# Kernel optimization log

Hardware: AMD Instinct MI355X
Metric: run time of the kernel (lower is better)

The kernel has to match this reference:

```python
import jax, jax.numpy as jnp
import numpy as np

VOC_SIZE = 100000
EMB_SIZE = 300
BATCH = 262144


def setup_inputs() -> dict:
    key = jax.random.key(0)
    k1, k2, k3, k4, k5, k6, k7, k8 = jax.random.split(key, 8)
    center = jax.random.randint(k1, (BATCH, 1), 0, VOC_SIZE)
    outside = jax.random.randint(k2, (BATCH, 1), 0, VOC_SIZE)
    coocs = jax.random.uniform(k3, (BATCH, 1), dtype=jnp.float32)
    weighting = jax.random.uniform(k4, (BATCH, 1), dtype=jnp.float32)
    center_embedding = jax.random.normal(k5, (VOC_SIZE, EMB_SIZE), dtype=jnp.float32)
    outside_embedding = jax.random.normal(k6, (VOC_SIZE, EMB_SIZE), dtype=jnp.float32)
    center_bias = jax.random.normal(k7, (VOC_SIZE, 1), dtype=jnp.float32)
    outside_bias = jax.random.normal(k8, (VOC_SIZE, 1), dtype=jnp.float32)
    return {
        "center": center,
        "outside": outside,
        "coocs": coocs,
        "weighting": weighting,
        "center_embedding": center_embedding,
        "outside_embedding": outside_embedding,
        "center_bias": center_bias,
        "outside_bias": outside_bias,
    }


def reference(center, outside, coocs, weighting,
              center_embedding, outside_embedding,
              center_bias, outside_bias):
    c_idx = center[:, 0]    # [B]
    o_idx = outside[:, 0]   # [B]
    center_embeds = center_embedding[c_idx]     # [B, E]
    outside_embeds = outside_embedding[o_idx]   # [B, E]
    c_bias = center_bias[c_idx]                 # [B, 1]
    o_bias = outside_bias[o_idx]                # [B, 1]
    # per-sample dot product, keepdims to match [B, 1]
    inner = jnp.sum(center_embeds * outside_embeds, axis=-1, keepdims=True)  # [B, 1]
    err = inner + c_bias + o_bias - coocs
    loss = jnp.sum(weighting * err * err)
    return loss
```

## Files before the change

### kernel.cpp

```cpp
#include <hip/hip_runtime.h>

#define BATCH 262144
#define EMB 300
#define NBLK 4096
#define WPB 4

__global__ __launch_bounds__(256) void glove_main(
    const int*   __restrict__ center,
    const int*   __restrict__ outside,
    const float* __restrict__ coocs,
    const float* __restrict__ weighting,
    const float* __restrict__ cemb,
    const float* __restrict__ oemb,
    const float* __restrict__ cbias,
    const float* __restrict__ obias,
    float*       __restrict__ block_sums)
{
    const int tid  = threadIdx.x;
    const int warp = tid >> 6;
    const int lane = tid & 63;
    const int l    = lane & 15;
    const int g    = lane >> 4;
    const int base = (blockIdx.x * WPB + warp) * 16 + g;

    int ci[4], oi[4];
    #pragma unroll
    for (int it = 0; it < 4; ++it) {
        ci[it] = center[base + it * 4];
        oi[it] = outside[base + it * 4];
    }

    float4 sa[2][5], sb[2][5];
    float  scb[2], sob[2], scc[2], swt[2];

    #pragma unroll
    for (int s = 0; s < 2; ++s) {
        const float4* __restrict__ A = (const float4*)(cemb + (long)ci[s] * EMB);
        const float4* __restrict__ B = (const float4*)(oemb + (long)oi[s] * EMB);
        #pragma unroll
        for (int i = 0; i < 4; ++i) {
            sa[s][i] = A[i * 16 + l];
            sb[s][i] = B[i * 16 + l];
        }
        sa[s][4].x = 0.f; sa[s][4].y = 0.f; sa[s][4].z = 0.f; sa[s][4].w = 0.f;
        sb[s][4] = sa[s][4];
        if (l < 11) {
            sa[s][4] = A[64 + l];
            sb[s][4] = B[64 + l];
        }
        scb[s] = cbias[ci[s]];
        sob[s] = obias[oi[s]];
        scc[s] = coocs[base + s * 4];
        swt[s] = weighting[base + s * 4];
    }

    float local = 0.0f;

    #pragma unroll
    for (int it = 0; it < 4; ++it) {
        const int buf = it & 1;

        float s = 0.f;
        #pragma unroll
        for (int i = 0; i < 5; ++i) {
            s += sa[buf][i].x * sb[buf][i].x + sa[buf][i].y * sb[buf][i].y
               + sa[buf][i].z * sb[buf][i].z + sa[buf][i].w * sb[buf][i].w;
        }
        const float cbv = scb[buf], obv = sob[buf], ccv = scc[buf], wtv = swt[buf];

        if (it + 2 < 4) {
            const int n = it + 2;
            const float4* __restrict__ A = (const float4*)(cemb + (long)ci[n] * EMB);
            const float4* __restrict__ B = (const float4*)(oemb + (long)oi[n] * EMB);
            #pragma unroll
            for (int i = 0; i < 4; ++i) {
                sa[buf][i] = A[i * 16 + l];
                sb[buf][i] = B[i * 16 + l];
            }
            if (l < 11) {
                sa[buf][4] = A[64 + l];
                sb[buf][4] = B[64 + l];
            } else {
                sa[buf][4].x = 0.f; sa[buf][4].y = 0.f; sa[buf][4].z = 0.f; sa[buf][4].w = 0.f;
                sb[buf][4] = sa[buf][4];
            }
            scb[buf] = cbias[ci[n]];
            sob[buf] = obias[oi[n]];
            scc[buf] = coocs[base + n * 4];
            swt[buf] = weighting[base + n * 4];
        }

        s += __shfl_xor(s, 1);
        s += __shfl_xor(s, 2);
        s += __shfl_xor(s, 4);
        s += __shfl_xor(s, 8);

        if (l == 0) {
            const float e = s + cbv + obv - ccv;
            local += wtv * e * e;
        }
    }

    local += __shfl_down(local, 32, 64);
    local += __shfl_down(local, 16, 64);

    __shared__ float smem[WPB];
    if (lane == 0) smem[warp] = local;
    __syncthreads();
    if (tid == 0)
        block_sums[blockIdx.x] = smem[0] + smem[1] + smem[2] + smem[3];
}

__global__ __launch_bounds__(1024) void glove_reduce(
    const float* __restrict__ part, float* __restrict__ out)
{
    const int t = threadIdx.x;
    float4 v = ((const float4*)part)[t];
    float s = v.x + v.y + v.z + v.w;
    #pragma unroll
    for (int off = 32; off > 0; off >>= 1)
        s += __shfl_down(s, off, 64);
    __shared__ float sm[16];
    if ((t & 63) == 0) sm[t >> 6] = s;
    __syncthreads();
    if (t < 16) {
        float x = sm[t];
        #pragma unroll
        for (int off = 8; off > 0; off >>= 1)
            x += __shfl_down(x, off, 16);
        if (t == 0) out[0] = x;
    }
}

extern "C" void kernel_launch(void* const* d_in, const int* in_sizes, int n_in,
                              void* d_out, int out_size, void* d_ws, size_t ws_size,
                              hipStream_t stream) {
    const int*   center    = (const int*)  d_in[0];
    const int*   outside   = (const int*)  d_in[1];
    const float* coocs     = (const float*)d_in[2];
    const float* weighting = (const float*)d_in[3];
    const float* cemb      = (const float*)d_in[4];
    const float* oemb      = (const float*)d_in[5];
    const float* cbias     = (const float*)d_in[6];
    const float* obias     = (const float*)d_in[7];
    float* out        = (float*)d_out;
    float* block_sums = (float*)d_ws;

    glove_main<<<NBLK, 256, 0, stream>>>(
        center, outside, coocs, weighting, cemb, oemb, cbias, obias, block_sums);
    glove_reduce<<<1, 1024, 0, stream>>>(block_sums, out);
}
```

Measured before the change: 302.8 us.

## Bucket-sort samples by center index to improve embedding gather locality

Adds a histogram, scan and atomic scatter pass that builds a permutation grouping samples by center-index bucket (128 rows per bucket). The main kernel then processes samples in that order, so center-embedding rows are likely reused from cache instead of being fetched randomly from DRAM. Each per-pair loss is written back to its original position and summed in original order, which keeps the reduction order fixed. In exchange it adds several extra launches, contended atomics within a bucket, and indirect loads of the index, cooc and weighting arrays. The outside-embedding gathers stay random.

Result: slower. 431.8 us (+42.6%).

```diff
diff --git a/kernel.cpp b/kernel.cpp
--- a/kernel.cpp
+++ b/kernel.cpp
@@ -2,8 +2,191 @@
 
 #define BATCH 262144
 #define EMB 300
+#define VOC 100000
 #define NBLK 4096
 #define WPB 4
+
+#define BSHIFT 7
+#define NBUCKET ((VOC + (1 << BSHIFT) - 1) >> BSHIFT)
+
+#define WS_BLOCKSUMS 0
+#define WS_HIST      16384
+#define WS_OFFS      20480
+#define WS_PERM      24576
+#define WS_PLOSS     (24576 + 1048576)
+#define WS_NEED      (WS_PLOSS + 1048576)
+
+__global__ __launch_bounds__(256) void glove_hist(
+    const int* __restrict__ center, int* __restrict__ hist)
+{
+    const int i = blockIdx.x * 256 + threadIdx.x;
+    atomicAdd(&hist[center[i] >> BSHIFT], 1);
+}
+
+__global__ __launch_bounds__(1024) void glove_scan(
+    const int* __restrict__ hist, int* __restrict__ offs)
+{
+    const int t = threadIdx.x;
+    int v = (t < NBUCKET) ? hist[t] : 0;
+    const int orig = v;
+
+    #pragma unroll
+    for (int off = 1; off < 64; off <<= 1) {
+        int n = __shfl_up(v, off, 64);
+        if ((t & 63) >= off) v += n;
+    }
+    __shared__ int wsums[16];
+    if ((t & 63) == 63) wsums[t >> 6] = v;
+    __syncthreads();
+    if (t < 16) {
+        int w = wsums[t];
+        #pragma unroll
+        for (int off = 1; off < 16; off <<= 1) {
+            int n = __shfl_up(w, off, 16);
+            if (t >= off) w += n;
+        }
+        wsums[t] = w;
+    }
+    __syncthreads();
+    const int add = (t >= 64) ? wsums[(t >> 6) - 1] : 0;
+    if (t < NBUCKET) offs[t] = (v + add) - orig;
+}
+
+__global__ __launch_bounds__(256) void glove_scatter(
+    const int* __restrict__ center, int* __restrict__ offs,
+    int* __restrict__ perm)
+{
+    const int i = blockIdx.x * 256 + threadIdx.x;
+    const int b = center[i] >> BSHIFT;
+    const int slot = atomicAdd(&offs[b], 1);
+    perm[slot] = i;
+}
+
+__global__ __launch_bounds__(256) void glove_main_perm(
+    const int*   __restrict__ perm,
+    const int*   __restrict__ center,
+    const int*   __restrict__ outside,
+    const float* __restrict__ coocs,
+    const float* __restrict__ weighting,
+    const float* __restrict__ cemb,
+    const float* __restrict__ oemb,
+    const float* __restrict__ cbias,
+    const float* __restrict__ obias,
+    float*       __restrict__ pair_loss)
+{
+    const int tid  = threadIdx.x;
+    const int warp = tid >> 6;
+    const int lane = tid & 63;
+    const int l    = lane & 15;
+    const int g    = lane >> 4;
+    const int base = (blockIdx.x * WPB + warp) * 16 + g;
+
+    int pp[4];
+    #pragma unroll
+    for (int it = 0; it < 4; ++it) pp[it] = perm[base + it * 4];
+
+    int ci[4], oi[4];
+    #pragma unroll
+    for (int it = 0; it < 4; ++it) {
+        ci[it] = center[pp[it]];
+        oi[it] = outside[pp[it]];
+    }
+
+    float4 sa[2][5], sb[2][5];
+    float  scb[2], sob[2], scc[2], swt[2];
+
+    #pragma unroll
+    for (int s = 0; s < 2; ++s) {
+        const float4* __restrict__ A = (const float4*)(cemb + (long)ci[s] * EMB);
+        const float4* __restrict__ B = (const float4*)(oemb + (long)oi[s] * EMB);
+        #pragma unroll
+        for (int i = 0; i < 4; ++i) {
+            sa[s][i] = A[i * 16 + l];
+            sb[s][i] = B[i * 16 + l];
+        }
+        sa[s][4].x = 0.f; sa[s][4].y = 0.f; sa[s][4].z = 0.f; sa[s][4].w = 0.f;
+        sb[s][4] = sa[s][4];
+        if (l < 11) {
+            sa[s][4] = A[64 + l];
+            sb[s][4] = B[64 + l];
+        }
+        scb[s] = cbias[ci[s]];
+        sob[s] = obias[oi[s]];
+        scc[s] = coocs[pp[s]];
+        swt[s] = weighting[pp[s]];
+    }
+
+    #pragma unroll
+    for (int it = 0; it < 4; ++it) {
+        const int buf = it & 1;
+
+        float s = 0.f;
+        #pragma unroll
+        for (int i = 0; i < 5; ++i) {
+            s += sa[buf][i].x * sb[buf][i].x + sa[buf][i].y * sb[buf][i].y
+               + sa[buf][i].z * sb[buf][i].z + sa[buf][i].w * sb[buf][i].w;
+        }
+        const float cbv = scb[buf], obv = sob[buf], ccv = scc[buf], wtv = swt[buf];
+
+        if (it + 2 < 4) {
+            const int n = it + 2;
+            const float4* __restrict__ A = (const float4*)(cemb + (long)ci[n] * EMB);
+            const float4* __restrict__ B = (const float4*)(oemb + (long)oi[n] * EMB);
+            #pragma unroll
+            for (int i = 0; i < 4; ++i) {
+                sa[buf][i] = A[i * 16 + l];
+                sb[buf][i] = B[i * 16 + l];
+            }
+            if (l < 11) {
+                sa[buf][4] = A[64 + l];
+                sb[buf][4] = B[64 + l];
+            } else {
+                sa[buf][4].x = 0.f; sa[buf][4].y = 0.f; sa[buf][4].z = 0.f; sa[buf][4].w = 0.f;
+                sb[buf][4] = sa[buf][4];
+            }
+            scb[buf] = cbias[ci[n]];
+            sob[buf] = obias[oi[n]];
+            scc[buf] = coocs[pp[n]];
+            swt[buf] = weighting[pp[n]];
+        }
+
+        s += __shfl_xor(s, 1);
+        s += __shfl_xor(s, 2);
+        s += __shfl_xor(s, 4);
+        s += __shfl_xor(s, 8);
+
+        if (l == 0) {
+            const float e = s + cbv + obv - ccv;
+            pair_loss[pp[it]] = wtv * e * e;
+        }
+    }
+}
+
+__global__ __launch_bounds__(256) void glove_sum(
+    const float* __restrict__ pair_loss, float* __restrict__ block_sums)
+{
+    const int tid  = threadIdx.x;
+    const int warp = tid >> 6;
+    const int lane = tid & 63;
+    const int l    = lane & 15;
+    const int g    = lane >> 4;
+    const int base = (blockIdx.x * WPB + warp) * 16 + g;
+
+    float local = 0.0f;
+    if (l == 0) {
+        #pragma unroll
+        for (int it = 0; it < 4; ++it)
+            local += pair_loss[base + it * 4];
+    }
+    local += __shfl_down(local, 32, 64);
+    local += __shfl_down(local, 16, 64);
+
+    __shared__ float smem[WPB];
+    if (lane == 0) smem[warp] = local;
+    __syncthreads();
+    if (tid == 0)
+        block_sums[blockIdx.x] = smem[0] + smem[1] + smem[2] + smem[3];
+}
 
 __global__ __launch_bounds__(256) void glove_main(
     const int*   __restrict__ center,
@@ -143,10 +326,28 @@
     const float* oemb      = (const float*)d_in[5];
     const float* cbias     = (const float*)d_in[6];
     const float* obias     = (const float*)d_in[7];
-    float* out        = (float*)d_out;
-    float* block_sums = (float*)d_ws;
-
-    glove_main<<<NBLK, 256, 0, stream>>>(
-        center, outside, coocs, weighting, cemb, oemb, cbias, obias, block_sums);
-    glove_reduce<<<1, 1024, 0, stream>>>(block_sums, out);
-}
+    float* out = (float*)d_out;
+
+    if (ws_size >= (size_t)WS_NEED) {
+        char*  ws         = (char*)d_ws;
+        float* block_sums = (float*)(ws + WS_BLOCKSUMS);
+        int*   hist       = (int*)  (ws + WS_HIST);
+        int*   offs       = (int*)  (ws + WS_OFFS);
+        int*   perm       = (int*)  (ws + WS_PERM);
+        float* ploss      = (float*)(ws + WS_PLOSS);
+
+        hipMemsetAsync(hist, 0, 4096, stream);
+        glove_hist   <<<BATCH / 256, 256, 0, stream>>>(center, hist);
+        glove_scan   <<<1, 1024, 0, stream>>>(hist, offs);
+        glove_scatter<<<BATCH / 256, 256, 0, stream>>>(center, offs, perm);
+        glove_main_perm<<<NBLK, 256, 0, stream>>>(
+            perm, center, outside, coocs, weighting, cemb, oemb, cbias, obias, ploss);
+        glove_sum    <<<NBLK, 256, 0, stream>>>(ploss, block_sums);
+        glove_reduce <<<1, 1024, 0, stream>>>(block_sums, out);
+    } else {
+        float* block_sums = (float*)d_ws;
+        glove_main  <<<NBLK, 256, 0, stream>>>(
+            center, outside, coocs, weighting, cemb, oemb, cbias, obias, block_sums);
+        glove_reduce<<<1, 1024, 0, stream>>>(block_sums, out);
+    }
+}
```
